# Performance work log

Hardware: AMD Instinct MI355X
Metric: run time of the kernel (lower is better)

## Reference

```python
import jax, jax.numpy as jnp
import numpy as np

D_MODEL = 512
KEY_DIM = 128
TEMP = 30.0          # RelationUnit temperature
EPS = 1e-5           # InstanceL2Norm eps
SCALE = float(np.sqrt(1.0 / (D_MODEL * 4 * 4)))  # norm_scale in layers


def _sine_pos(hw, d, dtype=jnp.float32):
    # pos_seq = ones(hw).cumsum() -> 1..hw; outer with inv_freq; cat(sin, cos)
    pos = jnp.arange(1, hw + 1, dtype=dtype)
    inv_freq = 1.0 / (10000.0 ** (jnp.arange(0, d, 2, dtype=dtype) / d))
    ang = pos[:, None] * inv_freq[None, :]          # [hw, d/2]
    return jnp.concatenate([jnp.sin(ang), jnp.cos(ang)], axis=-1)  # [hw, d]


def _attn(q, k, v, wk, bk):
    # Single-head RelationUnit: shared WK projection, L2-normalize, temp softmax, raw value.
    # q: [Lq,B,D], k,v: [Lk,B,D]
    pq = q @ wk.T + bk
    pq = pq / jnp.maximum(jnp.linalg.norm(pq, axis=-1, keepdims=True), 1e-12)
    pk = k @ wk.T + bk
    pk = pk / jnp.maximum(jnp.linalg.norm(pk, axis=-1, keepdims=True), 1e-12)
    logits = jnp.einsum('qbe,kbe->bqk', pq, pk) * TEMP   # [B,Lq,Lk]
    a = jax.nn.softmax(logits, axis=-1)
    return jnp.einsum('bqk,kbd->qbd', a, v)


def _inorm(x, ni, b, d, h, w):
    # InstanceL2Norm (size_average=True) over (d,h,w) per (ni,b) sample.
    y = x.reshape(ni, h, w, b, d)
    ss = jnp.sum(y * y, axis=(1, 2, 4), keepdims=True)
    y = y * (SCALE * jnp.sqrt((d * h * w) / (ss + EPS)))
    return y.reshape(ni * h * w, b, d)


def _flatten(x5):
    # (ni,b,d,h,w) -> (ni*h*w, b, d), matching torch view/permute/reshape order.
    ni, b, d, h, w = x5.shape
    return x5.reshape(ni, b, d, h * w).transpose(0, 3, 1, 2).reshape(ni * h * w, b, d)


def _encoder(src5, pos5, wk, bk):
    ni, b, d, h, w = src5.shape
    x = _flatten(src5) + _flatten(pos5) * 1e-3
    x = x + _attn(x, x, x, wk, bk)
    return _inorm(x, ni, b, d, h, w)


def _decoder_one(tgt5, pos5, memory, pos, wk_s, bk_s, wk_c, bk_c):
    # Single decoder layer on one image (ni == 1).
    ni, b, d, h, w = tgt5.shape
    x = _flatten(tgt5) + _flatten(pos5) * 1e-3
    x = x + _attn(x, x, x, wk_s, bk_s)
    x = _inorm(x, ni, b, d, h, w)
    mask = _attn(x, memory, pos, wk_c, bk_c)
    t2 = _inorm(x * mask, ni, b, d, h, w)
    t3 = _attn(x, memory, memory * pos, wk_c, bk_c)
    t4 = _inorm(x + t3, ni, b, d, h, w)
    x = _inorm(t2 + t4, ni, b, d, h, w)
    return x.reshape(ni, h, w, b, d).transpose(0, 3, 4, 1, 2).reshape(ni * b, d, h, w)


def _forward(train_feat, test_feat, train_label, wk_self, bk_self, wk_cross, bk_cross):
    ntr, b, d, h, w = train_feat.shape
    nte = test_feat.shape[0]
    # Sinusoidal position embedding, reshaped to (d,h,w), broadcast over imgs/batch.
    pe = _sine_pos(h * w, d, train_feat.dtype).reshape(h, w, d).transpose(2, 0, 1)
    train_pos = jnp.broadcast_to(pe, (ntr, b, d, h, w))
    test_pos = jnp.broadcast_to(pe, (nte, b, d, h, w))
    memory = _encoder(train_feat, train_pos, wk_self, bk_self)   # [ntr*h*w, b, d]
    # label -> pos value sequence [ntr*h*w, b, d] (repeated over channel dim)
    pos = train_label.reshape(ntr, b, 1, h * w).transpose(0, 3, 1, 2).reshape(ntr * h * w, b, 1)
    pos = jnp.broadcast_to(pos, (ntr * h * w, b, d))

    def dec(t4, p4):
        return _decoder_one(t4[None], p4[None], memory, pos,
                            wk_self, bk_self, wk_cross, bk_cross)

    enc_feat = jax.vmap(dec)(train_feat, train_pos).reshape(ntr * b, d, h, w)
    dec_feat = jax.vmap(dec)(test_feat, test_pos).reshape(nte * b, d, h, w)
    return enc_feat, dec_feat


def setup_inputs() -> dict:
    key = jax.random.key(0)
    k1, k2, k3, k4, k5 = jax.random.split(key, 5)
    NTR, NTE, B, D, H, W = 3, 3, 16, 512, 22, 22
    std = float(np.sqrt(2.0 / D))  # kaiming-like init for WK
    return {
        'train_feat': jax.random.normal(k1, (NTR, B, D, H, W), jnp.float32),
        'test_feat': jax.random.normal(k2, (NTE, B, D, H, W), jnp.float32),
        'train_label': jax.random.uniform(k3, (NTR, B, H, W), jnp.float32),
        'wk_self': jax.random.normal(k4, (KEY_DIM, D), jnp.float32) * std,
        'bk_self': jnp.zeros((KEY_DIM,), jnp.float32),
        'wk_cross': jax.random.normal(k5, (KEY_DIM, D), jnp.float32) * std,
        'bk_cross': jnp.zeros((KEY_DIM,), jnp.float32),
    }


def reference(train_feat, test_feat, train_label, wk_self, bk_self, wk_cross, bk_cross):
    return _forward(train_feat, test_feat, train_label,
                    wk_self, bk_self, wk_cross, bk_cross)
```

## Files before the change

kernel.cpp:

```cpp
#include <hip/hip_runtime.h>
#include <math.h>

#define BATCH   16
#define DMODEL  512
#define EKEY    128
#define HWSZ    484
#define LENC    1452
#define LKPAD   1536
#define IMG_ELEMS (HWSZ*BATCH*DMODEL)
#define ENC_OUT   11894784ull
#define SQRT_TEMP 5.4772255750516611f
#define INORM_SCALE 0.011048543456039806f
#define NEGBIG   -3.0e38f

typedef _Float16 f16;
typedef _Float16 f16x8 __attribute__((ext_vector_type(8)));
typedef _Float16 f16x4 __attribute__((ext_vector_type(4)));
typedef float    f32x4 __attribute__((ext_vector_type(4)));

__device__ __forceinline__ f32x4 mfma16(f16x8 a, f16x8 b, f32x4 c) {
  return __builtin_amdgcn_mfma_f32_16x16x32_f16(a, b, c, 0, 0, 0);
}
__device__ __forceinline__ float inorm_coef(float ss) {
  return INORM_SCALE * sqrtf(247808.0f / (ss + 1e-5f));
}

#define BARRIER() do { asm volatile("s_waitcnt lgkmcnt(0)" ::: "memory"); \
                       __builtin_amdgcn_s_barrier();                      \
                       asm volatile("" ::: "memory"); } while (0)

__device__ __forceinline__ size_t vfrag_addr(size_t z, int nkt, int d, int k) {
  return (((z * 32 + (d >> 4)) * (size_t)nkt + (k >> 5)) << 9)
         + (((k >> 3) & 3) << 7) + ((d & 15) << 3) + (k & 7);
}

__global__ void init_zero_kernel(float* __restrict__ ss) { ss[threadIdx.x] = 0.0f; }

__global__ void peT_kernel(float* __restrict__ peT) {
  const int c = blockIdx.x;
  const int cc = (c < 256) ? c : c - 256;
  const float invf = 1.0f / powf(10000.0f, (float)(2 * cc) * (1.0f / 512.0f));
  for (int p = threadIdx.x; p < HWSZ; p += blockDim.x) {
    const float ang = (float)(p + 1) * invf;
    peT[c * HWSZ + p] = (c < 256) ? sinf(ang) : cosf(ang);
  }
}

__global__ void build_labelT_kernel(const float* __restrict__ lab, float* __restrict__ labT) {
  const int g = blockIdx.x;
  if (g < 48) {
    const int im = g >> 4, b = g & 15;
    for (int p = threadIdx.x; p < HWSZ; p += blockDim.x)
      labT[(size_t)b * LKPAD + im * HWSZ + p] = lab[((size_t)im * BATCH + b) * HWSZ + p];
  } else {
    const int b = g - 48;
    for (int p = LENC + threadIdx.x; p < LKPAD; p += blockDim.x)
      labT[(size_t)b * LKPAD + p] = 0.0f;
  }
}

__global__ void cvt16_kernel(const float* __restrict__ s, f16* __restrict__ d) {
  const int i = (blockIdx.x * 256 + threadIdx.x) * 4;
  const int r = i >> 9, c = i & 511;
  const float4 v = *(const float4*)(s + i);
  f16x4 h; h[0] = (f16)v.x; h[1] = (f16)v.y; h[2] = (f16)v.z; h[3] = (f16)v.w;
  f16* dp = d + ((((size_t)(r >> 4) << 4) + (c >> 5)) << 9)
              + (((c >> 3) & 3) << 7) + ((r & 15) << 3) + (c & 7);
  *(f16x4*)dp = h;
}

__global__ void vpad_kernel(f16* __restrict__ vt) {
  const int d = blockIdx.x, b = blockIdx.y;
  const int k = LENC + threadIdx.x;
  if (k < LKPAD) vt[vfrag_addr(b, 48, d, k)] = (f16)0.f;
}

__global__ __launch_bounds__(256) void build_input_kernel(
    const float* __restrict__ trainf, const float* __restrict__ testf,
    const float* __restrict__ peT, int i0, float* __restrict__ xout,
    f16* __restrict__ vt, int zmul, int col_im_step, int nkt)
{
  __shared__ float tile[32][33];
  const int tx = threadIdx.x, ty = threadIdx.y;
  const int pt = blockIdx.x * 32, ct = blockIdx.y * 32;
  const int im = blockIdx.z >> 4, b = blockIdx.z & 15;
  const int g = i0 + im;
  const float* src = (g < 3 ? trainf + (size_t)g * IMG_ELEMS
                            : testf + (size_t)(g - 3) * IMG_ELEMS)
                     + (size_t)b * (512 * 484);
  const int zv = zmul ? (im * 16 + b) : b;
  const int col0 = im * col_im_step;
#pragma unroll
  for (int j = 0; j < 4; ++j) {
    const int c = ct + ty + 8 * j, p = pt + tx;
    const int k = col0 + p;
    float val = 0.0f;
    if (p < HWSZ) {
      val = src[(size_t)c * 484 + p] + 1e-3f * peT[(size_t)c * 484 + p];
      vt[vfrag_addr(zv, nkt, c, k)] = (f16)val;
    } else if (zmul) {
      vt[vfrag_addr(zv, nkt, c, k)] = (f16)0.f;
    }
    tile[ty + 8 * j][tx] = val;
  }
  __syncthreads();
#pragma unroll
  for (int j = 0; j < 4; ++j) {
    const int p = pt + ty + 8 * j, c = ct + tx;
    if (p < HWSZ)
      xout[(((size_t)im * HWSZ + p) * BATCH + b) * DMODEL + c] = tile[tx][ty + 8 * j];
  }
}

__global__ __launch_bounds__(256) void v16t_mem_kernel(
    const float* __restrict__ src, const float* __restrict__ ssE, f16* __restrict__ dst)
{
  __shared__ f16 tile[32][33];
  const int tx = threadIdx.x, ty = threadIdx.y;
  const int l0 = blockIdx.x * 32, d0 = blockIdx.y * 32;
  const int b = blockIdx.z;
#pragma unroll
  for (int j = 0; j < 4; ++j) {
    const int l = l0 + ty + 8 * j;
    float v = 0.0f;
    if (l < LENC) {
      const float cf = inorm_coef(ssE[(l / 484) * 16 + b]);
      v = cf * src[((size_t)l * BATCH + b) * DMODEL + d0 + tx];
    }
    tile[ty + 8 * j][tx] = (f16)v;
  }
  __syncthreads();
#pragma unroll
  for (int j = 0; j < 4; ++j) {
    const int d = d0 + ty + 8 * j, l = l0 + tx;
    if (l < LKPAD) dst[vfrag_addr(b, 48, d, l)] = tile[tx][ty + 8 * j];
  }
}

__global__ __launch_bounds__(256) void proj_mfma_kernel(
    const float* __restrict__ X, const f16* __restrict__ W16,
    const float* __restrict__ bias, const float* __restrict__ ssg,
    f16* __restrict__ P16, int L, int NLT)
{
  __shared__ f16 Xs[64][72];
  const int t = threadIdx.x;
  const int wave = t >> 6, lane = t & 63, quad = lane >> 4, ln = lane & 15;
  const int lane8 = lane * 8;
  const size_t row0 = (size_t)blockIdx.x * 64;

  f32x4 acc[8];
#pragma unroll
  for (int nt = 0; nt < 8; ++nt) acc[nt] = (f32x4){0.f, 0.f, 0.f, 0.f};

  const int sr = t >> 2, sko = (t & 3) * 16;
  const size_t rowg = row0 + sr;
  float cf = 1.0f;
  if (ssg) {
    const int bb = (int)(rowg & 15);
    const int gg = (int)((rowg >> 4) / 484);
    cf = inorm_coef(ssg[gg * 16 + bb]);
  }
  const float* xp = X + rowg * 512 + sko;

  for (int k0 = 0; k0 < 512; k0 += 64) {
    {
      const float4 a0 = *(const float4*)(xp + k0);
      const float4 a1 = *(const float4*)(xp + k0 + 4);
      const float4 a2 = *(const float4*)(xp + k0 + 8);
      const float4 a3 = *(const float4*)(xp + k0 + 12);
      f16x8 h0, h1;
      h0[0]=(f16)(cf*a0.x); h0[1]=(f16)(cf*a0.y); h0[2]=(f16)(cf*a0.z); h0[3]=(f16)(cf*a0.w);
      h0[4]=(f16)(cf*a1.x); h0[5]=(f16)(cf*a1.y); h0[6]=(f16)(cf*a1.z); h0[7]=(f16)(cf*a1.w);
      h1[0]=(f16)(cf*a2.x); h1[1]=(f16)(cf*a2.y); h1[2]=(f16)(cf*a2.z); h1[3]=(f16)(cf*a2.w);
      h1[4]=(f16)(cf*a3.x); h1[5]=(f16)(cf*a3.y); h1[6]=(f16)(cf*a3.z); h1[7]=(f16)(cf*a3.w);
      *(f16x8*)&Xs[sr][sko]     = h0;
      *(f16x8*)&Xs[sr][sko + 8] = h1;
    }
    __syncthreads();
#pragma unroll
    for (int ks = 0; ks < 2; ++ks) {
      const f16x8 a = *(const f16x8*)&Xs[wave * 16 + ln][ks * 32 + quad * 8];
      const int kt = (k0 >> 5) + ks;
#pragma unroll
      for (int nt = 0; nt < 8; ++nt) {
        const f16x8 bf = *(const f16x8*)(W16 + (((size_t)(nt * 16 + kt)) << 9) + lane8);
        acc[nt] = mfma16(a, bf, acc[nt]);
      }
    }
    __syncthreads();
  }

  float bj[8];
#pragma unroll
  for (int nt = 0; nt < 8; ++nt) bj[nt] = bias[nt * 16 + ln];

  float y[8][4]; float ssq[4] = {0.f, 0.f, 0.f, 0.f};
#pragma unroll
  for (int nt = 0; nt < 8; ++nt)
#pragma unroll
    for (int r = 0; r < 4; ++r) {
      const float v = acc[nt][r] + bj[nt];
      y[nt][r] = v; ssq[r] = fmaf(v, v, ssq[r]);
    }
#pragma unroll
  for (int r = 0; r < 4; ++r) {
    ssq[r] += __shfl_xor(ssq[r], 1); ssq[r] += __shfl_xor(ssq[r], 2);
    ssq[r] += __shfl_xor(ssq[r], 4); ssq[r] += __shfl_xor(ssq[r], 8);
  }
#pragma unroll
  for (int r = 0; r < 4; ++r) {
    const float inv = SQRT_TEMP / fmaxf(sqrtf(ssq[r]), 1e-12f);
    const size_t rg = row0 + (size_t)wave * 16 + quad * 4 + r;
    const int b = (int)(rg & 15);
    const size_t lg = rg >> 4;
    const int im = (int)(lg / (size_t)L);
    const int l  = (int)(lg - (size_t)im * L);
    f16* zb = P16 + (((size_t)(im * 16 + b) * NLT + (l >> 4)) << 11) + ((l & 15) << 3) + (ln & 7);
#pragma unroll
    for (int nt = 0; nt < 8; ++nt)
      zb[((size_t)(nt >> 1) << 9) + (((nt * 2 + (ln >> 3)) & 3) << 7)] = (f16)(y[nt][r] * inv);
  }
}

template<int CROSS>
__global__ __launch_bounds__(512) void attn6_kernel(
    const f16* __restrict__ pq, const f16* __restrict__ pk, const f16* __restrict__ Vt,
    const float* __restrict__ labT, float* __restrict__ X, float* __restrict__ Vout,
    const float* __restrict__ ssIn, float* __restrict__ ssO,
    float* __restrict__ ssV_, float* __restrict__ ssUV_,
    int Lq, int Lk, int nqb, int nltq, int nltk, int nktv, int pk_shared, int vt_shared)
{
  __shared__ float Ssm[64][132];
  __shared__ f16   Psm[64][136];
  __shared__ float msh[64], lsh[64], ash[64], mask_sh[64];

  const int t = threadIdx.x;
  const int wave = t >> 6, lane = t & 63, quad = lane >> 4, ln = lane & 15;
  const int lane8 = lane * 8;

  const int id = blockIdx.x;
  const int b  = (id & 7) + 8 * ((id >> 3) & 1);
  const int jj = id >> 4;
  const int qb = jj % nqb, im = jj / nqb;
  const int q0 = qb * 64;
  const int zq = im * 16 + b;
  const int zk = pk_shared ? b : zq;
  const int zv = vt_shared ? b : zq;

  const f16* pqz = pq + (((size_t)zq * nltq) << 11);
  const f16* pkz = pk + (((size_t)zk * nltk) << 11);
  const f16* Vw  = Vt + ((((size_t)zv * 32 + wave * 4) * (size_t)nktv) << 9) + lane8;
  const float* ksb = CROSS ? labT + (size_t)b * LKPAD : (const float*)0;

  f16x8 qf[4][4];
#pragma unroll
  for (int mt = 0; mt < 4; ++mt) {
    const f16* qp = pqz + (((size_t)((q0 >> 4) + mt)) << 11) + lane8;
#pragma unroll
    for (int es = 0; es < 4; ++es) qf[mt][es] = *(const f16x8*)(qp + es * 512);
  }
  f16x8 kf[4];
  {
    const f16* kp = pkz + (((size_t)wave) << 11) + lane8;
#pragma unroll
    for (int es = 0; es < 4; ++es) kf[es] = *(const f16x8*)(kp + es * 512);
  }

  f32x4 oacc[4][4];
#pragma unroll
  for (int mt = 0; mt < 4; ++mt)
#pragma unroll
    for (int nt = 0; nt < 4; ++nt) oacc[mt][nt] = (f32x4){0.f, 0.f, 0.f, 0.f};

  if (t < 64) { msh[t] = NEGBIG; lsh[t] = 0.f; ash[t] = 0.f; }
  float msum = 0.f;
  const int qs = t >> 3, cs = t & 7;
  __syncthreads();

  const int nch = (Lk + 127) >> 7;

  for (int ch = 0; ch < nch; ++ch) {
    const int k0 = ch << 7;
    const int ktb = k0 >> 5;
    f16x8 bvA[4], bvB[4];
#pragma unroll
    for (int nt = 0; nt < 4; ++nt) {
      const f16* vpn = Vw + (((size_t)nt * nktv + ktb) << 9);
      bvA[nt] = *(const f16x8*)(vpn);
      bvB[nt] = *(const f16x8*)(vpn + 512);
    }
    float4 lv[4];
    if (CROSS) {
      const float* lp = ksb + k0 + cs * 16;
#pragma unroll
      for (int i = 0; i < 4; ++i) lv[i] = *(const float4*)(lp + i * 4);
    }
    {
      f32x4 s[4];
#pragma unroll
      for (int mt = 0; mt < 4; ++mt) s[mt] = (f32x4){0.f,0.f,0.f,0.f};
#pragma unroll
      for (int es = 0; es < 4; ++es)
#pragma unroll
        for (int mt = 0; mt < 4; ++mt)
          s[mt] = mfma16(qf[mt][es], kf[es], s[mt]);
#pragma unroll
      for (int mt = 0; mt < 4; ++mt)
#pragma unroll
        for (int r = 0; r < 4; ++r)
          Ssm[mt * 16 + quad * 4 + r][wave * 16 + ln] = s[mt][r];
    }
    if (ch + 1 < nch) {
      const f16* kp = pkz + (((size_t)(((ch + 1) << 3) + wave)) << 11) + lane8;
#pragma unroll
      for (int es = 0; es < 4; ++es) kf[es] = *(const f16x8*)(kp + es * 512);
    }
    BARRIER();
    {
      f32x4 sa[4];
#pragma unroll
      for (int i = 0; i < 4; ++i) sa[i] = *(const f32x4*)&Ssm[qs][cs * 16 + i * 4];
      const int kb = k0 + cs * 16;
      float sv[16];
#pragma unroll
      for (int i = 0; i < 4; ++i)
#pragma unroll
        for (int j = 0; j < 4; ++j)
          sv[i * 4 + j] = (kb + i * 4 + j < Lk) ? sa[i][j] : NEGBIG;
      float mx = sv[0];
#pragma unroll
      for (int j = 1; j < 16; ++j) mx = fmaxf(mx, sv[j]);
      mx = fmaxf(mx, __shfl_xor(mx, 1));
      mx = fmaxf(mx, __shfl_xor(mx, 2));
      mx = fmaxf(mx, __shfl_xor(mx, 4));
      const float mold = msh[qs];
      const float mnew = fmaxf(mold, mx);
      const float alpha = __expf(mold - mnew);
      float ps = 0.f, pm = 0.f;
      f16x8 pv0, pv1;
#pragma unroll
      for (int j = 0; j < 16; ++j) {
        float p = __expf(sv[j] - mnew);
        ps += p;
        if (CROSS) p *= lv[j >> 2][j & 3];
        pm += p;
        if (j < 8) pv0[j] = (f16)p; else pv1[j - 8] = (f16)p;
      }
      *(f16x8*)&Psm[qs][cs * 16]     = pv0;
      *(f16x8*)&Psm[qs][cs * 16 + 8] = pv1;
      ps += __shfl_xor(ps, 1); ps += __shfl_xor(ps, 2); ps += __shfl_xor(ps, 4);
      msum = msum * alpha + pm;
      if (cs == 0) { msh[qs] = mnew; lsh[qs] = lsh[qs] * alpha + ps; ash[qs] = alpha; }
    }
    BARRIER();
    {
      f16x8 bvC[4];
#pragma unroll
      for (int nt = 0; nt < 4; ++nt)
        bvC[nt] = *(const f16x8*)(Vw + (((size_t)nt * nktv + ktb + 2) << 9));
#pragma unroll
      for (int mt = 0; mt < 4; ++mt) {
        f32x4 al;
#pragma unroll
        for (int r = 0; r < 4; ++r) al[r] = ash[mt * 16 + quad * 4 + r];
#pragma unroll
        for (int nt = 0; nt < 4; ++nt) oacc[mt][nt] *= al;
      }
      f16x8 pa[4];
#pragma unroll
      for (int mt = 0; mt < 4; ++mt) pa[mt] = *(const f16x8*)&Psm[mt * 16 + ln][quad * 8];
#pragma unroll
      for (int nt = 0; nt < 4; ++nt)
#pragma unroll
        for (int mt = 0; mt < 4; ++mt)
          oacc[mt][nt] = mfma16(pa[mt], bvA[nt], oacc[mt][nt]);
      f16x8 bvD[4];
#pragma unroll
      for (int nt = 0; nt < 4; ++nt)
        bvD[nt] = *(const f16x8*)(Vw + (((size_t)nt * nktv + ktb + 3) << 9));
#pragma unroll
      for (int mt = 0; mt < 4; ++mt) pa[mt] = *(const f16x8*)&Psm[mt * 16 + ln][32 + quad * 8];
#pragma unroll
      for (int nt = 0; nt < 4; ++nt)
#pragma unroll
        for (int mt = 0; mt < 4; ++mt)
          oacc[mt][nt] = mfma16(pa[mt], bvB[nt], oacc[mt][nt]);
#pragma unroll
      for (int mt = 0; mt < 4; ++mt) pa[mt] = *(const f16x8*)&Psm[mt * 16 + ln][64 + quad * 8];
#pragma unroll
      for (int nt = 0; nt < 4; ++nt)
#pragma unroll
        for (int mt = 0; mt < 4; ++mt)
          oacc[mt][nt] = mfma16(pa[mt], bvC[nt], oacc[mt][nt]);
#pragma unroll
      for (int mt = 0; mt < 4; ++mt) pa[mt] = *(const f16x8*)&Psm[mt * 16 + ln][96 + quad * 8];
#pragma unroll
      for (int nt = 0; nt < 4; ++nt)
#pragma unroll
        for (int mt = 0; mt < 4; ++mt)
          oacc[mt][nt] = mfma16(pa[mt], bvD[nt], oacc[mt][nt]);
    }
  }

  if (CROSS) {
    float ms = msum;
    ms += __shfl_xor(ms, 1); ms += __shfl_xor(ms, 2); ms += __shfl_xor(ms, 4);
    if (cs == 0) mask_sh[qs] = ms / lsh[qs];
    __syncthreads();
  }

  const int g0  = (im * Lq + q0) / 484;
  const int bhi = (g0 + 1) * 484 - im * Lq;
  const bool strad = (!CROSS) && (bhi < Lq) && (bhi < q0 + 64);

  float a0 = 0.f, a1 = 0.f, a2 = 0.f;
  const float cfA = CROSS ? inorm_coef(ssIn[im * 16 + b]) : 0.f;

#pragma unroll
  for (int mt = 0; mt < 4; ++mt) {
    f32x4 li;
#pragma unroll
    for (int r = 0; r < 4; ++r) li[r] = 1.0f / lsh[mt * 16 + quad * 4 + r];
#pragma unroll
    for (int r = 0; r < 4; ++r) {
      const int q = q0 + mt * 16 + quad * 4 + r;
      if (q < Lq) {
        const size_t base = (((size_t)(im * Lq + q)) * BATCH + b) * DMODEL + wave * 64 + ln;
        if (!CROSS) {
          const bool hi = (q >= bhi);
#pragma unroll
          for (int nt = 0; nt < 4; ++nt) {
            const float y = X[base + nt * 16] + oacc[mt][nt][r] * li[r];
            X[base + nt * 16] = y;
            if (hi) a1 += y * y; else a0 += y * y;
          }
        } else {
          const float mval = mask_sh[mt * 16 + quad * 4 + r];
#pragma unroll
          for (int nt = 0; nt < 4; ++nt) {
            const float x1 = cfA * X[base + nt * 16];
            const float u = x1 * mval;
            const float v = x1 + oacc[mt][nt][r] * li[r];
            X[base + nt * 16] = u;
            Vout[base + nt * 16] = v;
            a0 += u * u; a1 += v * v; a2 += u * v;
          }
        }
      }
    }
  }
#pragma unroll
  for (int m = 32; m; m >>= 1) {
    a0 += __shfl_xor(a0, m); a1 += __shfl_xor(a1, m);
    if (CROSS) a2 += __shfl_xor(a2, m);
  }
  if (lane == 0) {
    if (!CROSS) {
      atomicAdd(ssO + g0 * 16 + b, a0);
      if (strad) atomicAdd(ssO + (g0 + 1) * 16 + b, a1);
    } else {
      const int g = im * 16 + b;
      atomicAdd(ssO + g, a0);
      atomicAdd(ssV_ + g, a1);
      atomicAdd(ssUV_ + g, a2);
    }
  }
}

__global__ void coef_final_kernel(const float* __restrict__ ssU, const float* __restrict__ ssV,
                                  const float* __restrict__ ssUV, float* __restrict__ AB, int n)
{
  const int t = threadIdx.x;
  if (t < n) {
    const float su = ssU[t], sv = ssV[t], suv = ssUV[t];
    const float cu = inorm_coef(su), cv = inorm_coef(sv);
    const float ssz = cu * cu * su + cv * cv * sv + 2.f * cu * cv * suv;
    const float cz = inorm_coef(ssz);
    AB[2 * t] = cu * cz; AB[2 * t + 1] = cv * cz;
  }
}

__global__ __launch_bounds__(256) void final_out_kernel(
    const float* __restrict__ u, const float* __restrict__ v,
    const float* __restrict__ AB, float* __restrict__ out, int i0)
{
  __shared__ float tile[32][33];
  const int tx = threadIdx.x, ty = threadIdx.y;
  const int pt = blockIdx.x * 32, ct = blockIdx.y * 32;
  const int z = blockIdx.z;
  const int im = z >> 4, b = z & 15;
  const float A = AB[2 * z], B = AB[2 * z + 1];
#pragma unroll
  for (int j = 0; j < 4; ++j) {
    const int p = pt + ty + 8 * j, c = ct + tx;
    float val = 0.0f;
    if (p < HWSZ) {
      const size_t idx = (((size_t)im * HWSZ + p) * BATCH + b) * DMODEL + c;
      val = A * u[idx] + B * v[idx];
    }
    tile[ty + 8 * j][tx] = val;
  }
  __syncthreads();
  const int g = i0 + im;
  const size_t base = (g < 3 ? 0ull : ENC_OUT)
                    + ((size_t)(((g < 3 ? g : g - 3) * 16 + b) * 512)) * 484ull;
#pragma unroll
  for (int j = 0; j < 4; ++j) {
    const int c = ct + ty + 8 * j, p = pt + tx;
    if (p < HWSZ) out[base + (size_t)c * 484 + p] = tile[tx][ty + 8 * j];
  }
}

extern "C" void kernel_launch(void* const* d_in, const int* in_sizes, int n_in,
                              void* d_out, int out_size, void* d_ws, size_t ws_size,
                              hipStream_t stream) {
  (void)in_sizes; (void)n_in; (void)out_size;
  const float* train_feat  = (const float*)d_in[0];
  const float* test_feat   = (const float*)d_in[1];
  const float* train_label = (const float*)d_in[2];
  const float* wk_self     = (const float*)d_in[3];
  const float* bk_self     = (const float*)d_in[4];
  const float* wk_cross    = (const float*)d_in[5];
  const float* bk_cross    = (const float*)d_in[6];
  float* out = (float*)d_out;
  char* wsb  = (char*)d_ws;

  size_t off = 0;
  auto alloc = [&](size_t bytes) { size_t r = off; off = (r + bytes + 255) & ~(size_t)255; return r; };
  const size_t o_peT   = alloc(991232ull);
  const size_t o_labT  = alloc(16ull * LKPAD * 4);
  const size_t o_ss    = alloc(4096);
  const size_t o_w16s  = alloc(131072);
  const size_t o_w16c  = alloc(131072);
  const size_t o_xenc  = alloc(47579136ull);
  const size_t o_p16   = alloc(6291456ull);
  const size_t o_vte   = alloc(16ull*512*LKPAD*2);
  const size_t o_vtm   = alloc(16ull*512*LKPAD*2);
  const size_t fixed = off;

  float* peT  = (float*)(wsb + o_peT);
  float* labT = (float*)(wsb + o_labT);
  float* ss   = (float*)(wsb + o_ss);
  f16*   w16s = (f16*)(wsb + o_w16s);
  f16*   w16c = (f16*)(wsb + o_w16c);
  float* xenc = (float*)(wsb + o_xenc);
  f16*   p16  = (f16*)(wsb + o_p16);
  f16*   vte  = (f16*)(wsb + o_vte);
  f16*   vtm  = (f16*)(wsb + o_vtm);
  float* ssE = ss, *ssA = ss + 128, *ssU = ss + 256, *ssV = ss + 384, *ssUV = ss + 512;
  float* AB  = ss + 640;

  const size_t decPer = 15859712ull * 2 + 2097152ull + 8388608ull;
  int NB = 6;
  if (fixed + (size_t)NB * decPer + 4096 > ws_size) NB = 3;
  if (fixed + (size_t)NB * decPer + 4096 > ws_size) NB = 1;

  float* xd    = (float*)(wsb + fixed);
  float* vbuf  = xd + (size_t)NB * IMG_ELEMS;
  f16*   pq16d = (f16*)(vbuf + (size_t)NB * IMG_ELEMS);
  f16*   vtd   = pq16d + (size_t)NB * 1048576ull;

  init_zero_kernel<<<dim3(1), dim3(1024), 0, stream>>>(ss);
  peT_kernel<<<dim3(512), dim3(256), 0, stream>>>(peT);
  build_labelT_kernel<<<dim3(64), dim3(256), 0, stream>>>(train_label, labT);
  cvt16_kernel<<<dim3(64), dim3(256), 0, stream>>>(wk_self, w16s);
  cvt16_kernel<<<dim3(64), dim3(256), 0, stream>>>(wk_cross, w16c);
  vpad_kernel<<<dim3(512, 16), dim3(96), 0, stream>>>(vte);

  build_input_kernel<<<dim3(16, 16, 48), dim3(32, 8), 0, stream>>>(
      train_feat, test_feat, peT, 0, xenc, vte, 0, 484, 48);
  proj_mfma_kernel<<<dim3(363), dim3(256), 0, stream>>>(xenc, w16s, bk_self, (const float*)0, p16, LENC, 96);
  attn6_kernel<0><<<dim3(23 * 16), dim3(512), 0, stream>>>(
      p16, p16, vte, (const float*)0, xenc, (float*)0, (const float*)0,
      ssE, (float*)0, (float*)0, LENC, LENC, 23, 96, 96, 48, 0, 0);
  proj_mfma_kernel<<<dim3(363), dim3(256), 0, stream>>>(xenc, w16c, bk_cross, ssE, p16, LENC, 96);
  v16t_mem_kernel<<<dim3(48, 16, 16), dim3(32, 8), 0, stream>>>(xenc, ssE, vtm);

  for (int i0 = 0; i0 < 6; i0 += NB) {
    build_input_kernel<<<dim3(16, 16, NB * 16), dim3(32, 8), 0, stream>>>(
        train_feat, test_feat, peT, i0, xd, vtd, 1, 0, 16);
    proj_mfma_kernel<<<dim3(NB * 121), dim3(256), 0, stream>>>(xd, w16s, bk_self, (const float*)0, pq16d, HWSZ, 32);
    attn6_kernel<0><<<dim3(8 * 16 * NB), dim3(512), 0, stream>>>(
        pq16d, pq16d, vtd, (const float*)0, xd, (float*)0, (const float*)0,
        ssA + i0 * 16, (float*)0, (float*)0, HWSZ, HWSZ, 8, 32, 32, 16, 0, 0);
    proj_mfma_kernel<<<dim3(NB * 121), dim3(256), 0, stream>>>(xd, w16c, bk_cross, ssA + i0 * 16, pq16d, HWSZ, 32);
    attn6_kernel<1><<<dim3(8 * 16 * NB), dim3(512), 0, stream>>>(
        pq16d, p16 , vtm, labT, xd, vbuf, ssA + i0 * 16,
        ssU + i0 * 16, ssV + i0 * 16, ssUV + i0 * 16, HWSZ, LENC, 8, 32, 96, 48, 1, 1);
    coef_final_kernel<<<dim3(1), dim3(128), 0, stream>>>(
        ssU + i0 * 16, ssV + i0 * 16, ssUV + i0 * 16, AB + i0 * 32, NB * 16);
    final_out_kernel<<<dim3(16, 16, NB * 16), dim3(32, 8), 0, stream>>>(
        xd, vbuf, AB + i0 * 32, out, i0);
  }
}
```

Before: 916.7 us.

## Software-pipeline global loads in projection and attention kernels, add MFMA priority hints

The projection kernel now loads the next 64-column slice of X into registers before the barrier, so the fetch overlaps the MFMA work on the current slice. The attention kernel loads V fragments one chunk ahead: A/B for the next chunk are fetched during the current chunk's PV step, and C/D at the start of each chunk. s_setprio raises wave priority around MFMA bursts, and the softmax bounds mask now runs only on the tail chunk, with a tree-shaped max reduction. These changes aim to hide global-load latency, at the cost of more live registers and possible occupancy pressure.

```diff
diff --git a/kernel.cpp b/kernel.cpp
--- a/kernel.cpp
+++ b/kernel.cpp
@@ -162,12 +162,13 @@
   }
   const float* xp = X + rowg * 512 + sko;
 
+  float4 a0 = *(const float4*)(xp);
+  float4 a1 = *(const float4*)(xp + 4);
+  float4 a2 = *(const float4*)(xp + 8);
+  float4 a3 = *(const float4*)(xp + 12);
+
   for (int k0 = 0; k0 < 512; k0 += 64) {
     {
-      const float4 a0 = *(const float4*)(xp + k0);
-      const float4 a1 = *(const float4*)(xp + k0 + 4);
-      const float4 a2 = *(const float4*)(xp + k0 + 8);
-      const float4 a3 = *(const float4*)(xp + k0 + 12);
       f16x8 h0, h1;
       h0[0]=(f16)(cf*a0.x); h0[1]=(f16)(cf*a0.y); h0[2]=(f16)(cf*a0.z); h0[3]=(f16)(cf*a0.w);
       h0[4]=(f16)(cf*a1.x); h0[5]=(f16)(cf*a1.y); h0[6]=(f16)(cf*a1.z); h0[7]=(f16)(cf*a1.w);
@@ -176,18 +177,26 @@
       *(f16x8*)&Xs[sr][sko]     = h0;
       *(f16x8*)&Xs[sr][sko + 8] = h1;
     }
-    __syncthreads();
+    if (k0 + 64 < 512) {
+      a0 = *(const float4*)(xp + k0 + 64);
+      a1 = *(const float4*)(xp + k0 + 68);
+      a2 = *(const float4*)(xp + k0 + 72);
+      a3 = *(const float4*)(xp + k0 + 76);
+    }
+    BARRIER();
 #pragma unroll
     for (int ks = 0; ks < 2; ++ks) {
       const f16x8 a = *(const f16x8*)&Xs[wave * 16 + ln][ks * 32 + quad * 8];
       const int kt = (k0 >> 5) + ks;
+      __builtin_amdgcn_s_setprio(1);
 #pragma unroll
       for (int nt = 0; nt < 8; ++nt) {
         const f16x8 bf = *(const f16x8*)(W16 + (((size_t)(nt * 16 + kt)) << 9) + lane8);
         acc[nt] = mfma16(a, bf, acc[nt]);
       }
-    }
-    __syncthreads();
+      __builtin_amdgcn_s_setprio(0);
+    }
+    BARRIER();
   }
 
   float bj[8];
@@ -223,7 +232,7 @@
 }
 
 template<int CROSS>
-__global__ __launch_bounds__(512) void attn6_kernel(
+__global__ __launch_bounds__(512) void attn7_kernel(
     const f16* __restrict__ pq, const f16* __restrict__ pk, const f16* __restrict__ Vt,
     const float* __restrict__ labT, float* __restrict__ X, float* __restrict__ Vout,
     const float* __restrict__ ssIn, float* __restrict__ ssO,
@@ -265,6 +274,13 @@
 #pragma unroll
     for (int es = 0; es < 4; ++es) kf[es] = *(const f16x8*)(kp + es * 512);
   }
+  f16x8 bvA[4], bvB[4];
+#pragma unroll
+  for (int nt = 0; nt < 4; ++nt) {
+    const f16* vpn = Vw + (((size_t)nt * nktv) << 9);
+    bvA[nt] = *(const f16x8*)(vpn);
+    bvB[nt] = *(const f16x8*)(vpn + 512);
+  }
 
   f32x4 oacc[4][4];
 #pragma unroll
@@ -282,12 +298,12 @@
   for (int ch = 0; ch < nch; ++ch) {
     const int k0 = ch << 7;
     const int ktb = k0 >> 5;
-    f16x8 bvA[4], bvB[4];
+    f16x8 bvC[4], bvD[4];
 #pragma unroll
     for (int nt = 0; nt < 4; ++nt) {
-      const f16* vpn = Vw + (((size_t)nt * nktv + ktb) << 9);
-      bvA[nt] = *(const f16x8*)(vpn);
-      bvB[nt] = *(const f16x8*)(vpn + 512);
+      const f16* vpn = Vw + (((size_t)(nt * nktv + ktb + 2)) << 9);
+      bvC[nt] = *(const f16x8*)(vpn);
+      bvD[nt] = *(const f16x8*)(vpn + 512);
     }
     float4 lv[4];
     if (CROSS) {
@@ -299,11 +315,13 @@
       f32x4 s[4];
 #pragma unroll
       for (int mt = 0; mt < 4; ++mt) s[mt] = (f32x4){0.f,0.f,0.f,0.f};
+      __builtin_amdgcn_s_setprio(1);
 #pragma unroll
       for (int es = 0; es < 4; ++es)
 #pragma unroll
         for (int mt = 0; mt < 4; ++mt)
           s[mt] = mfma16(qf[mt][es], kf[es], s[mt]);
+      __builtin_amdgcn_s_setprio(0);
 #pragma unroll
       for (int mt = 0; mt < 4; ++mt)
 #pragma unroll
@@ -320,16 +338,25 @@
       f32x4 sa[4];
 #pragma unroll
       for (int i = 0; i < 4; ++i) sa[i] = *(const f32x4*)&Ssm[qs][cs * 16 + i * 4];
-      const int kb = k0 + cs * 16;
       float sv[16];
 #pragma unroll
       for (int i = 0; i < 4; ++i)
 #pragma unroll
         for (int j = 0; j < 4; ++j)
-          sv[i * 4 + j] = (kb + i * 4 + j < Lk) ? sa[i][j] : NEGBIG;
-      float mx = sv[0];
-#pragma unroll
-      for (int j = 1; j < 16; ++j) mx = fmaxf(mx, sv[j]);
+          sv[i * 4 + j] = sa[i][j];
+      if (k0 + 128 > Lk) {
+        const int kb = k0 + cs * 16;
+#pragma unroll
+        for (int j = 0; j < 16; ++j)
+          if (kb + j >= Lk) sv[j] = NEGBIG;
+      }
+      float m8[8];
+#pragma unroll
+      for (int j = 0; j < 8; ++j) m8[j] = fmaxf(sv[j], sv[j + 8]);
+      float m4[4];
+#pragma unroll
+      for (int j = 0; j < 4; ++j) m4[j] = fmaxf(m8[j], m8[j + 4]);
+      float mx = fmaxf(fmaxf(m4[0], m4[2]), fmaxf(m4[1], m4[3]));
       mx = fmaxf(mx, __shfl_xor(mx, 1));
       mx = fmaxf(mx, __shfl_xor(mx, 2));
       mx = fmaxf(mx, __shfl_xor(mx, 4));
@@ -354,10 +381,6 @@
     }
     BARRIER();
     {
-      f16x8 bvC[4];
-#pragma unroll
-      for (int nt = 0; nt < 4; ++nt)
-        bvC[nt] = *(const f16x8*)(Vw + (((size_t)nt * nktv + ktb + 2) << 9));
 #pragma unroll
       for (int mt = 0; mt < 4; ++mt) {
         f32x4 al;
@@ -369,36 +392,48 @@
       f16x8 pa[4];
 #pragma unroll
       for (int mt = 0; mt < 4; ++mt) pa[mt] = *(const f16x8*)&Psm[mt * 16 + ln][quad * 8];
+      __builtin_amdgcn_s_setprio(1);
 #pragma unroll
       for (int nt = 0; nt < 4; ++nt)
 #pragma unroll
         for (int mt = 0; mt < 4; ++mt)
           oacc[mt][nt] = mfma16(pa[mt], bvA[nt], oacc[mt][nt]);
-      f16x8 bvD[4];
-#pragma unroll
-      for (int nt = 0; nt < 4; ++nt)
-        bvD[nt] = *(const f16x8*)(Vw + (((size_t)nt * nktv + ktb + 3) << 9));
+      __builtin_amdgcn_s_setprio(0);
 #pragma unroll
       for (int mt = 0; mt < 4; ++mt) pa[mt] = *(const f16x8*)&Psm[mt * 16 + ln][32 + quad * 8];
+      __builtin_amdgcn_s_setprio(1);
 #pragma unroll
       for (int nt = 0; nt < 4; ++nt)
 #pragma unroll
         for (int mt = 0; mt < 4; ++mt)
           oacc[mt][nt] = mfma16(pa[mt], bvB[nt], oacc[mt][nt]);
+      __builtin_amdgcn_s_setprio(0);
+      if (ch + 1 < nch) {
+#pragma unroll
+        for (int nt = 0; nt < 4; ++nt) {
+          const f16* vpn = Vw + (((size_t)(nt * nktv + ktb + 4)) << 9);
+          bvA[nt] = *(const f16x8*)(vpn);
+          bvB[nt] = *(const f16x8*)(vpn + 512);
+        }
+      }
 #pragma unroll
       for (int mt = 0; mt < 4; ++mt) pa[mt] = *(const f16x8*)&Psm[mt * 16 + ln][64 + quad * 8];
+      __builtin_amdgcn_s_setprio(1);
 #pragma unroll
       for (int nt = 0; nt < 4; ++nt)
 #pragma unroll
         for (int mt = 0; mt < 4; ++mt)
           oacc[mt][nt] = mfma16(pa[mt], bvC[nt], oacc[mt][nt]);
+      __builtin_amdgcn_s_setprio(0);
 #pragma unroll
       for (int mt = 0; mt < 4; ++mt) pa[mt] = *(const f16x8*)&Psm[mt * 16 + ln][96 + quad * 8];
+      __builtin_amdgcn_s_setprio(1);
 #pragma unroll
       for (int nt = 0; nt < 4; ++nt)
 #pragma unroll
         for (int mt = 0; mt < 4; ++mt)
           oacc[mt][nt] = mfma16(pa[mt], bvD[nt], oacc[mt][nt]);
+      __builtin_amdgcn_s_setprio(0);
     }
   }
 
@@ -570,7 +605,7 @@
   build_input_kernel<<<dim3(16, 16, 48), dim3(32, 8), 0, stream>>>(
       train_feat, test_feat, peT, 0, xenc, vte, 0, 484, 48);
   proj_mfma_kernel<<<dim3(363), dim3(256), 0, stream>>>(xenc, w16s, bk_self, (const float*)0, p16, LENC, 96);
-  attn6_kernel<0><<<dim3(23 * 16), dim3(512), 0, stream>>>(
+  attn7_kernel<0><<<dim3(23 * 16), dim3(512), 0, stream>>>(
       p16, p16, vte, (const float*)0, xenc, (float*)0, (const float*)0,
       ssE, (float*)0, (float*)0, LENC, LENC, 23, 96, 96, 48, 0, 0);
   proj_mfma_kernel<<<dim3(363), dim3(256), 0, stream>>>(xenc, w16c, bk_cross, ssE, p16, LENC, 96);
@@ -580,11 +615,11 @@
     build_input_kernel<<<dim3(16, 16, NB * 16), dim3(32, 8), 0, stream>>>(
         train_feat, test_feat, peT, i0, xd, vtd, 1, 0, 16);
     proj_mfma_kernel<<<dim3(NB * 121), dim3(256), 0, stream>>>(xd, w16s, bk_self, (const float*)0, pq16d, HWSZ, 32);
-    attn6_kernel<0><<<dim3(8 * 16 * NB), dim3(512), 0, stream>>>(
+    attn7_kernel<0><<<dim3(8 * 16 * NB), dim3(512), 0, stream>>>(
         pq16d, pq16d, vtd, (const float*)0, xd, (float*)0, (const float*)0,
         ssA + i0 * 16, (float*)0, (float*)0, HWSZ, HWSZ, 8, 32, 32, 16, 0, 0);
     proj_mfma_kernel<<<dim3(NB * 121), dim3(256), 0, stream>>>(xd, w16c, bk_cross, ssA + i0 * 16, pq16d, HWSZ, 32);
-    attn6_kernel<1><<<dim3(8 * 16 * NB), dim3(512), 0, stream>>>(
+    attn7_kernel<1><<<dim3(8 * 16 * NB), dim3(512), 0, stream>>>(
         pq16d, p16 , vtm, labT, xd, vbuf, ssA + i0 * 16,
         ssU + i0 * 16, ssV + i0 * 16, ssUV + i0 * 16, HWSZ, LENC, 8, 32, 96, 48, 1, 1);
     coef_final_kernel<<<dim3(1), dim3(128), 0, stream>>>(
```

Measured after the change: 1.098 ms. 19.7% more time.
